# Kernel tuning notes

Measured on AMD Instinct MI355X. Metric: run time of the kernel, lower is better.

Reference implementation:

```python
import jax, jax.numpy as jnp
import numpy as np

B, IN, OUT, K = 16384, 2048, 2048, 8
P, Q = OUT // K, IN // K
W_BIT, IN_BIT = 8, 8
V_MAX = 2.0
ACT_THRES = 6.0


def _ste(base, quantized):
    # straight-through estimator: forward = quantized, backward = d(base)
    return base + jax.lax.stop_gradient(quantized - base)


def quantize_input(x, in_bit):
    # unsigned uniform quantization of activations into [0, 1]
    levels = float(2 ** in_bit - 1)
    xc = jnp.clip(x, 0.0, 1.0)
    xq = jnp.round(xc * levels) / levels
    return _ste(xc, xq)


def quantize_weight(w, w_bit, v_max):
    # symmetric uniform quantization into [-v_max, v_max]
    s = float(2 ** (w_bit - 1) - 1)
    wc = jnp.clip(w, -v_max, v_max)
    wq = jnp.round(wc / v_max * s) / s * v_max
    return _ste(wc, wq)


def setup_inputs() -> dict:
    key = jax.random.key(0)
    k1, k2 = jax.random.split(key)
    x = jax.random.uniform(k1, (B, IN), dtype=jnp.float32)
    weight = jax.random.normal(k2, (P, Q, K, K), dtype=jnp.float32) * 0.1
    return {"x": x, "weight": weight}


def reference(x, weight):
    xq = quantize_input(x, IN_BIT)                    # [B, IN]
    wq = quantize_weight(weight, W_BIT, V_MAX)        # [P, Q, K, K]
    xb = xq.reshape(x.shape[0], Q, K)                 # [B, Q, K]
    # blocked matmul: out[b,p,o] = sum_q sum_i W[p,q,o,i] * x[b,q,i]
    out = jnp.einsum("bqi,pqoi->bpo", xb, wq).reshape(x.shape[0], OUT)
    out = out * out                                   # photodetect: intensity |.|^2
    out = jnp.clip(out, 0.0, ACT_THRES)               # ReLUN(6)
    return out
```

## Files before the change

### kernel.cpp

```cpp
#include <hip/hip_runtime.h>
#include <stdint.h>


typedef int i32x4 __attribute__((ext_vector_type(4)));

#define B_DIM   16384
#define IN_DIM  2048
#define OUT_DIM 2048

#define BM 256
#define BN 256
#define BK 64
#define KTILES (IN_DIM / BK)
#define BUFB   (2 * BM * BK)

__device__ __forceinline__ void async16(const void* g, void* l) {
    __builtin_amdgcn_global_load_lds(
        (const __attribute__((address_space(1))) void*)g,
        (__attribute__((address_space(3))) void*)l, 16, 0, 0);
}

__global__ __launch_bounds__(256) void quant_x_kernel(const float* __restrict__ x,
                                                      int8_t* __restrict__ xq) {
    int i = blockIdx.x * 256 + threadIdx.x;
    const float4* xv = (const float4*)x + (size_t)i * 4;
    union { int8_t c[16]; i32x4 v; } u;
#pragma unroll
    for (int j = 0; j < 4; ++j) {
        float4 v = xv[j];
        float f[4] = {v.x, v.y, v.z, v.w};
#pragma unroll
        for (int e = 0; e < 4; ++e) {
            float c = fminf(fmaxf(f[e], 0.0f), 1.0f);
            int q = (int)rintf(c * 255.0f) - 128;
            u.c[j * 4 + e] = (int8_t)q;
        }
    }
    *((i32x4*)xq + i) = u.v;
}

__global__ __launch_bounds__(256) void quant_w_kernel(const float* __restrict__ w,
                                                      int8_t* __restrict__ wq,
                                                      int* __restrict__ rowsum) {
    int p = blockIdx.x;
    int t = threadIdx.x;
    const float* wp = w + (size_t)p * 16384;
    int n = p * 8 + (t & 7);
    int lsum = 0;
#pragma unroll
    for (int s = 0; s < 8; ++s) {
        int g = t + s * 256;
        float4 v0 = *(const float4*)(wp + g * 8);
        float4 v1 = *(const float4*)(wp + g * 8 + 4);
        float f[8] = {v0.x, v0.y, v0.z, v0.w, v1.x, v1.y, v1.z, v1.w};
        union { int8_t c[8]; long long ll; } u;
#pragma unroll
        for (int e = 0; e < 8; ++e) {
            float c = fminf(fmaxf(f[e], -2.0f), 2.0f);
            int q = (int)rintf(c * 63.5f);
            u.c[e] = (int8_t)q;
            lsum += q;
        }
        int kg = g >> 3;
        *(long long*)(wq + (size_t)n * 2048 + kg * 8) = u.ll;
    }
    atomicAdd(&rowsum[n], lsum);
}

__global__ __launch_bounds__(512, 2) void gemm_i8_kernel(const int8_t* __restrict__ A,
                                                         const int8_t* __restrict__ W,
                                                         const int* __restrict__ rowsum,
                                                         float* __restrict__ out) {
    extern __shared__ int8_t lds[];

    int bid = blockIdx.x;
    int wg = (bid & 7) * 64 + (bid >> 3);
    int tm = wg >> 3;
    int tn = wg & 7;
    int brow = tm * BM;
    int bcol = tn * BN;

    int tid  = threadIdx.x;
    int lane = tid & 63;
    int wv   = tid >> 6;
    int wr = wv >> 2, wc = wv & 3;
    int l15 = lane & 15;
    int kg  = lane >> 4;

    int r0 = tid >> 2;
    int c0 = tid & 3;
    int sw = ((c0 ^ ((r0 >> 1) & 3)) << 4);
    const int8_t* gA0 = A + (size_t)(brow + r0) * IN_DIM + sw;
    const int8_t* gA1 = A + (size_t)(brow + r0 + 128) * IN_DIM + sw;
    const int8_t* gB0 = W + (size_t)(bcol + r0) * IN_DIM + sw;
    const int8_t* gB1 = W + (size_t)(bcol + r0 + 128) * IN_DIM + sw;
    const int ldsOff = tid * 16;

    const int koff = ((kg ^ ((l15 >> 1) & 3)) << 4);
    const int aoff = (wr * 128 + l15) * BK + koff;
    const int boff = (wc * 64 + l15) * BK + koff;

    i32x4 acc[8][4];
#pragma unroll
    for (int m = 0; m < 8; ++m)
#pragma unroll
        for (int n = 0; n < 4; ++n)
            acc[m][n] = (i32x4){0, 0, 0, 0};

    auto stage = [&](int bi, int kt) {
        int8_t* la = lds + bi * BUFB;
        int8_t* lb = la + BM * BK;
        const int kb = kt * BK;
        async16(gA0 + kb, la + ldsOff);
        async16(gA1 + kb, la + ldsOff + 8192);
        async16(gB0 + kb, lb + ldsOff);
        async16(gB1 + kb, lb + ldsOff + 8192);
    };

    auto compute = [&](int bi) {
        const int8_t* la = lds + bi * BUFB;
        const int8_t* lb = la + BM * BK;
        i32x4 af[8], bf[4];
#pragma unroll
        for (int m = 0; m < 8; ++m)
            af[m] = *(const i32x4*)(la + aoff + m * (16 * BK));
#pragma unroll
        for (int n = 0; n < 4; ++n)
            bf[n] = *(const i32x4*)(lb + boff + n * (16 * BK));
#pragma unroll
        for (int m = 0; m < 8; ++m)
#pragma unroll
            for (int n = 0; n < 4; ++n)
                acc[m][n] = __builtin_amdgcn_mfma_i32_16x16x64_i8(af[m], bf[n],
                                                                  acc[m][n], 0, 0, 0);
    };

    stage(0, 0);
    stage(1, 1);

    for (int kt = 0; kt < KTILES - 2; ++kt) {
        asm volatile("s_waitcnt vmcnt(4)" ::: "memory");
        __builtin_amdgcn_s_barrier();
        __builtin_amdgcn_sched_barrier(0);
        stage((kt + 2) % 3, kt + 2);
        compute(kt % 3);
    }
    asm volatile("s_waitcnt vmcnt(4)" ::: "memory");
    __builtin_amdgcn_s_barrier();
    __builtin_amdgcn_sched_barrier(0);
    compute((KTILES - 2) % 3);
    asm volatile("s_waitcnt vmcnt(0)" ::: "memory");
    __builtin_amdgcn_s_barrier();
    __builtin_amdgcn_sched_barrier(0);
    compute((KTILES - 1) % 3);

    const float scale = (float)(2.0 / 32385.0);
#pragma unroll
    for (int n = 0; n < 4; ++n) {
        int col = bcol + wc * 64 + n * 16 + l15;
        int rs128 = rowsum[col] << 7;
#pragma unroll
        for (int m = 0; m < 8; ++m) {
            int row0 = brow + wr * 128 + m * 16 + kg * 4;
#pragma unroll
            for (int r = 0; r < 4; ++r) {
                float f = (float)(acc[m][n][r] + rs128) * scale;
                f = f * f;
                f = fminf(f, 6.0f);
                out[(size_t)(row0 + r) * OUT_DIM + col] = f;
            }
        }
    }
}

extern "C" void kernel_launch(void* const* d_in, const int* in_sizes, int n_in,
                              void* d_out, int out_size, void* d_ws, size_t ws_size,
                              hipStream_t stream) {
    const float* x  = (const float*)d_in[0];
    const float* wt = (const float*)d_in[1];
    float* out = (float*)d_out;

    char* ws = (char*)d_ws;
    int8_t* xq = (int8_t*)ws;
    int8_t* wq = (int8_t*)(ws + (size_t)B_DIM * IN_DIM);
    int*    rowsum = (int*)(ws + (size_t)B_DIM * IN_DIM
                               + (size_t)OUT_DIM * IN_DIM);

    hipMemsetAsync(rowsum, 0, OUT_DIM * sizeof(int), stream);
    quant_x_kernel<<<(B_DIM * IN_DIM / 16) / 256, 256, 0, stream>>>(x, xq);
    quant_w_kernel<<<256, 256, 0, stream>>>(wt, wq, rowsum);
    gemm_i8_kernel<<<(B_DIM / BM) * (OUT_DIM / BN), 512, 3 * BUFB, stream>>>(xq, wq, rowsum, out);
}
```

Before: 125.2 us.

## Split each K-tile into two phases, interleaving LDS reads, async loads and MFMAs

Restructures the int8 GEMM main loop into a ping-pong style schedule. Each K-tile is computed in two halves: A/B fragments for the first half are read, the A prefetch is issued, then MFMAs run at raised priority, followed by the second half with the B prefetch. The loop is unrolled by three to make buffer indices compile-time constants. This is meant to overlap LDS reads and global loads with matrix math and to cut fragment register pressure, at the cost of extra barriers per tile.

```diff
diff --git a/kernel.cpp b/kernel.cpp
--- a/kernel.cpp
+++ b/kernel.cpp
@@ -67,6 +67,59 @@
     atomicAdd(&rowsum[n], lsum);
 }
 
+#define MFMA_I8(a, b, c) __builtin_amdgcn_mfma_i32_16x16x64_i8(a, b, c, 0, 0, 0)
+
+#define DO_TILE(BI, KT2, STG, WAITN) do {                                     \
+    int8_t* la = lds + (BI) * BUFB;                                           \
+    int8_t* lb = la + BM * BK;                                                \
+    int8_t* ldst = lds + (((BI) + 2) % 3) * BUFB;                             \
+            \
+    _Pragma("unroll")                                                         \
+    for (int m = 0; m < 4; ++m)                                               \
+        af[m] = *(const i32x4*)(la + aoff + m * 1024);                        \
+    _Pragma("unroll")                                                         \
+    for (int n = 0; n < 4; ++n)                                               \
+        bf[n] = *(const i32x4*)(lb + boff + n * 1024);                        \
+    if (STG) { const int kb = (KT2) * BK;                                     \
+        async16(gA0 + kb, ldst + ldsOff);                                     \
+        async16(gA1 + kb, ldst + ldsOff + 8192); }                            \
+    __builtin_amdgcn_sched_barrier(0);                                        \
+    __builtin_amdgcn_s_barrier();                                             \
+    asm volatile("s_waitcnt lgkmcnt(0)" ::: "memory");                        \
+    __builtin_amdgcn_sched_barrier(0);                                        \
+    __builtin_amdgcn_s_setprio(1);                                            \
+    _Pragma("unroll")                                                         \
+    for (int m = 0; m < 4; ++m)                                               \
+        _Pragma("unroll")                                                     \
+        for (int n = 0; n < 4; ++n)                                           \
+            acc[m][n] = MFMA_I8(af[m], bf[n], acc[m][n]);                     \
+    __builtin_amdgcn_s_setprio(0);                                            \
+    __builtin_amdgcn_sched_barrier(0);                                        \
+    __builtin_amdgcn_s_barrier();                                             \
+                  \
+    _Pragma("unroll")                                                         \
+    for (int m = 4; m < 8; ++m)                                               \
+        af[m] = *(const i32x4*)(la + aoff + m * 1024);                        \
+    if (STG) { const int kb = (KT2) * BK;                                     \
+        async16(gB0 + kb, ldst + BM * BK + ldsOff);                           \
+        async16(gB1 + kb, ldst + BM * BK + ldsOff + 8192); }                  \
+    __builtin_amdgcn_sched_barrier(0);                                        \
+    __builtin_amdgcn_s_barrier();                                             \
+    asm volatile("s_waitcnt lgkmcnt(0)" ::: "memory");                        \
+    __builtin_amdgcn_sched_barrier(0);                                        \
+    __builtin_amdgcn_s_setprio(1);                                            \
+    _Pragma("unroll")                                                         \
+    for (int m = 4; m < 8; ++m)                                               \
+        _Pragma("unroll")                                                     \
+        for (int n = 0; n < 4; ++n)                                           \
+            acc[m][n] = MFMA_I8(af[m], bf[n], acc[m][n]);                     \
+    __builtin_amdgcn_s_setprio(0);                                            \
+    __builtin_amdgcn_sched_barrier(0);                                        \
+    if ((WAITN) == 4)      asm volatile("s_waitcnt vmcnt(4)" ::: "memory");   \
+    else if ((WAITN) == 0) asm volatile("s_waitcnt vmcnt(0)" ::: "memory");   \
+    if ((WAITN) >= 0) __builtin_amdgcn_s_barrier();                           \
+} while (0)
+
 __global__ __launch_bounds__(512, 2) void gemm_i8_kernel(const int8_t* __restrict__ A,
                                                          const int8_t* __restrict__ W,
                                                          const int* __restrict__ rowsum,
@@ -106,53 +159,29 @@
 #pragma unroll
         for (int n = 0; n < 4; ++n)
             acc[m][n] = (i32x4){0, 0, 0, 0};
-
-    auto stage = [&](int bi, int kt) {
-        int8_t* la = lds + bi * BUFB;
-        int8_t* lb = la + BM * BK;
-        const int kb = kt * BK;
-        async16(gA0 + kb, la + ldsOff);
-        async16(gA1 + kb, la + ldsOff + 8192);
-        async16(gB0 + kb, lb + ldsOff);
-        async16(gB1 + kb, lb + ldsOff + 8192);
-    };
-
-    auto compute = [&](int bi) {
-        const int8_t* la = lds + bi * BUFB;
-        const int8_t* lb = la + BM * BK;
-        i32x4 af[8], bf[4];
-#pragma unroll
-        for (int m = 0; m < 8; ++m)
-            af[m] = *(const i32x4*)(la + aoff + m * (16 * BK));
-#pragma unroll
-        for (int n = 0; n < 4; ++n)
-            bf[n] = *(const i32x4*)(lb + boff + n * (16 * BK));
-#pragma unroll
-        for (int m = 0; m < 8; ++m)
-#pragma unroll
-            for (int n = 0; n < 4; ++n)
-                acc[m][n] = __builtin_amdgcn_mfma_i32_16x16x64_i8(af[m], bf[n],
-                                                                  acc[m][n], 0, 0, 0);
-    };
-
-    stage(0, 0);
-    stage(1, 1);
-
-    for (int kt = 0; kt < KTILES - 2; ++kt) {
-        asm volatile("s_waitcnt vmcnt(4)" ::: "memory");
-        __builtin_amdgcn_s_barrier();
-        __builtin_amdgcn_sched_barrier(0);
-        stage((kt + 2) % 3, kt + 2);
-        compute(kt % 3);
-    }
+    i32x4 af[8], bf[4];
+
+    async16(gA0, lds + ldsOff);
+    async16(gA1, lds + ldsOff + 8192);
+    async16(gB0, lds + BM * BK + ldsOff);
+    async16(gB1, lds + BM * BK + ldsOff + 8192);
+    async16(gA0 + BK, lds + BUFB + ldsOff);
+    async16(gA1 + BK, lds + BUFB + ldsOff + 8192);
+    async16(gB0 + BK, lds + BUFB + BM * BK + ldsOff);
+    async16(gB1 + BK, lds + BUFB + BM * BK + ldsOff + 8192);
     asm volatile("s_waitcnt vmcnt(4)" ::: "memory");
     __builtin_amdgcn_s_barrier();
-    __builtin_amdgcn_sched_barrier(0);
-    compute((KTILES - 2) % 3);
-    asm volatile("s_waitcnt vmcnt(0)" ::: "memory");
-    __builtin_amdgcn_s_barrier();
-    __builtin_amdgcn_sched_barrier(0);
-    compute((KTILES - 1) % 3);
+
+    int kt = 0;
+#pragma unroll 1
+    for (int t = 0; t < 10; ++t) {
+        DO_TILE(0, kt + 2, 1, 4);
+        DO_TILE(1, kt + 3, 1, 4);
+        DO_TILE(2, kt + 4, 1, 4);
+        kt += 3;
+    }
+    DO_TILE(0, 0, 0, 0);
+    DO_TILE(1, 0, 0, -1);
 
     const float scale = (float)(2.0 / 32385.0);
 #pragma unroll
```

After: 123.1 us. About the same (-1.7%).

## Fuse activation quantization into int8 GEMM A-tile loading with interleaved MFMA schedule

Applied to the files above, without the earlier changes.

Removes the separate x-quantization kernel. The GEMM now loads fp32 activations into registers, quantizes them to int8 in-kernel and writes them to LDS. Weight tiles still arrive through async global-to-LDS loads. The main loop is also restructured: LDS fragment reads are interleaved with MFMA groups under explicit waitcnts, the MFMA section runs at raised wave priority, and the loop is unrolled over three buffers. This avoids the extra int8 round trip through memory and one launch, but each column tile now re-reads fp32 activations, which is four times the bytes per tile, and the extra VALU quantization work competes with the MFMAs.

```diff
diff --git a/kernel.cpp b/kernel.cpp
--- a/kernel.cpp
+++ b/kernel.cpp
@@ -12,7 +12,8 @@
 #define BN 256
 #define BK 64
 #define KTILES (IN_DIM / BK)
-#define BUFB   (2 * BM * BK)
+#define ATILE  (BM * BK)
+#define BUFB   (2 * ATILE)
 
 __device__ __forceinline__ void async16(const void* g, void* l) {
     __builtin_amdgcn_global_load_lds(
@@ -20,23 +21,12 @@
         (__attribute__((address_space(3))) void*)l, 16, 0, 0);
 }
 
-__global__ __launch_bounds__(256) void quant_x_kernel(const float* __restrict__ x,
-                                                      int8_t* __restrict__ xq) {
-    int i = blockIdx.x * 256 + threadIdx.x;
-    const float4* xv = (const float4*)x + (size_t)i * 4;
-    union { int8_t c[16]; i32x4 v; } u;
-#pragma unroll
-    for (int j = 0; j < 4; ++j) {
-        float4 v = xv[j];
-        float f[4] = {v.x, v.y, v.z, v.w};
-#pragma unroll
-        for (int e = 0; e < 4; ++e) {
-            float c = fminf(fmaxf(f[e], 0.0f), 1.0f);
-            int q = (int)rintf(c * 255.0f) - 128;
-            u.c[j * 4 + e] = (int8_t)q;
-        }
-    }
-    *((i32x4*)xq + i) = u.v;
+__device__ __forceinline__ int q4(float4 v) {
+    int a = (int)rintf(fminf(fmaxf(v.x, 0.f), 1.f) * 255.f) - 128;
+    int b = (int)rintf(fminf(fmaxf(v.y, 0.f), 1.f) * 255.f) - 128;
+    int c = (int)rintf(fminf(fmaxf(v.z, 0.f), 1.f) * 255.f) - 128;
+    int d = (int)rintf(fminf(fmaxf(v.w, 0.f), 1.f) * 255.f) - 128;
+    return (a & 255) | ((b & 255) << 8) | ((c & 255) << 16) | ((d & 255) << 24);
 }
 
 __global__ __launch_bounds__(256) void quant_w_kernel(const float* __restrict__ w,
@@ -67,7 +57,73 @@
     atomicAdd(&rowsum[n], lsum);
 }
 
-__global__ __launch_bounds__(512, 2) void gemm_i8_kernel(const int8_t* __restrict__ A,
+#define SB0 __builtin_amdgcn_sched_barrier(0)
+#define WLG(n) asm volatile("s_waitcnt lgkmcnt(" #n ")" ::: "memory")
+#define WVM(n) asm volatile("s_waitcnt vmcnt(" #n ")" ::: "memory")
+
+#define CL(mm)                                                                \
+    _Pragma("unroll")                                                         \
+    for (int n = 0; n < 4; ++n)                                               \
+        acc[mm][n] = __builtin_amdgcn_mfma_i32_16x16x64_i8(af[mm], bf[n],     \
+                                                           acc[mm][n], 0, 0, 0);
+
+#define DO_TILE(BI, KT2, STG, TAILW) do {                                     \
+    const int8_t* la = lds + (BI) * BUFB;                                     \
+    const int8_t* lb = la + ATILE;                                            \
+    int8_t* dst = lds + (((BI) + 2) % 3) * BUFB;                              \
+    if (STG) {            \
+        const float* g0 = gx0 + (size_t)(KT2) * BK;                           \
+        const float* g1 = gx1 + (size_t)(KT2) * BK;                           \
+        fa0 = *(const float4*)(g0);       fa1 = *(const float4*)(g0 + 4);     \
+        fa2 = *(const float4*)(g0 + 8);   fa3 = *(const float4*)(g0 + 12);    \
+        fa4 = *(const float4*)(g1);       fa5 = *(const float4*)(g1 + 4);     \
+        fa6 = *(const float4*)(g1 + 8);   fa7 = *(const float4*)(g1 + 12);    \
+    }                                                                         \
+    SB0;                                                                      \
+    if (STG) {            \
+        async16(gB0 + (KT2) * BK, dst + ATILE + ldsOff);                      \
+        async16(gB1 + (KT2) * BK, dst + ATILE + ldsOff + 8192);               \
+    }                                                                         \
+    SB0;                                                                      \
+    bf[0] = *(const i32x4*)(lb + boff);                                       \
+    bf[1] = *(const i32x4*)(lb + boff + 1024);                                \
+    bf[2] = *(const i32x4*)(lb + boff + 2048);                                \
+    bf[3] = *(const i32x4*)(lb + boff + 3072);                                \
+    af[0] = *(const i32x4*)(la + aoff);                                       \
+    SB0;                                                                      \
+    af[1] = *(const i32x4*)(la + aoff + 1024);                                \
+    af[2] = *(const i32x4*)(la + aoff + 2048);                                \
+    SB0;                                                                      \
+    __builtin_amdgcn_s_setprio(1);                                            \
+    WLG(2); SB0; CL(0);                                                       \
+    af[3] = *(const i32x4*)(la + aoff + 3072); SB0;                           \
+    WLG(2); SB0; CL(1);                                                       \
+    af[4] = *(const i32x4*)(la + aoff + 4096); SB0;                           \
+    WLG(2); SB0; CL(2);                                                       \
+    af[5] = *(const i32x4*)(la + aoff + 5120); SB0;                           \
+    WLG(2); SB0; CL(3);                                                       \
+    af[6] = *(const i32x4*)(la + aoff + 6144); SB0;                           \
+    WLG(2); SB0; CL(4);                                                       \
+    af[7] = *(const i32x4*)(la + aoff + 7168); SB0;                           \
+    WLG(2); SB0; CL(5);                                                       \
+    WLG(1); SB0; CL(6);                                                       \
+    WLG(0); SB0; CL(7);                                                       \
+    __builtin_amdgcn_s_setprio(0);                                            \
+    SB0;                                                                      \
+    if (STG) {            \
+        WVM(2); SB0;                                                          \
+        i32x4 pk0, pk1;                                                       \
+        pk0[0] = q4(fa0); pk0[1] = q4(fa1); pk0[2] = q4(fa2); pk0[3] = q4(fa3);\
+        pk1[0] = q4(fa4); pk1[1] = q4(fa5); pk1[2] = q4(fa6); pk1[3] = q4(fa7);\
+        *(i32x4*)(dst + ldsOff) = pk0;                                        \
+        *(i32x4*)(dst + ldsOff + 8192) = pk1;                                 \
+    }                                                                         \
+    if ((TAILW) == 0) { WVM(0); }                                             \
+    WLG(0);                                                                   \
+    __builtin_amdgcn_s_barrier();                                             \
+} while (0)
+
+__global__ __launch_bounds__(512, 2) void gemm_i8_kernel(const float* __restrict__ X,
                                                          const int8_t* __restrict__ W,
                                                          const int* __restrict__ rowsum,
                                                          float* __restrict__ out) {
@@ -90,8 +146,8 @@
     int r0 = tid >> 2;
     int c0 = tid & 3;
     int sw = ((c0 ^ ((r0 >> 1) & 3)) << 4);
-    const int8_t* gA0 = A + (size_t)(brow + r0) * IN_DIM + sw;
-    const int8_t* gA1 = A + (size_t)(brow + r0 + 128) * IN_DIM + sw;
+    const float*  gx0 = X + (size_t)(brow + r0) * IN_DIM + sw;
+    const float*  gx1 = X + (size_t)(brow + r0 + 128) * IN_DIM + sw;
     const int8_t* gB0 = W + (size_t)(bcol + r0) * IN_DIM + sw;
     const int8_t* gB1 = W + (size_t)(bcol + r0 + 128) * IN_DIM + sw;
     const int ldsOff = tid * 16;
@@ -106,53 +162,53 @@
 #pragma unroll
         for (int n = 0; n < 4; ++n)
             acc[m][n] = (i32x4){0, 0, 0, 0};
-
-    auto stage = [&](int bi, int kt) {
-        int8_t* la = lds + bi * BUFB;
-        int8_t* lb = la + BM * BK;
-        const int kb = kt * BK;
-        async16(gA0 + kb, la + ldsOff);
-        async16(gA1 + kb, la + ldsOff + 8192);
-        async16(gB0 + kb, lb + ldsOff);
-        async16(gB1 + kb, lb + ldsOff + 8192);
-    };
-
-    auto compute = [&](int bi) {
-        const int8_t* la = lds + bi * BUFB;
-        const int8_t* lb = la + BM * BK;
-        i32x4 af[8], bf[4];
-#pragma unroll
-        for (int m = 0; m < 8; ++m)
-            af[m] = *(const i32x4*)(la + aoff + m * (16 * BK));
-#pragma unroll
-        for (int n = 0; n < 4; ++n)
-            bf[n] = *(const i32x4*)(lb + boff + n * (16 * BK));
-#pragma unroll
-        for (int m = 0; m < 8; ++m)
-#pragma unroll
-            for (int n = 0; n < 4; ++n)
-                acc[m][n] = __builtin_amdgcn_mfma_i32_16x16x64_i8(af[m], bf[n],
-                                                                  acc[m][n], 0, 0, 0);
-    };
-
-    stage(0, 0);
-    stage(1, 1);
-
-    for (int kt = 0; kt < KTILES - 2; ++kt) {
-        asm volatile("s_waitcnt vmcnt(4)" ::: "memory");
-        __builtin_amdgcn_s_barrier();
-        __builtin_amdgcn_sched_barrier(0);
-        stage((kt + 2) % 3, kt + 2);
-        compute(kt % 3);
-    }
-    asm volatile("s_waitcnt vmcnt(4)" ::: "memory");
+    i32x4 af[8], bf[4];
+    float4 fa0, fa1, fa2, fa3, fa4, fa5, fa6, fa7;
+
+    fa0 = *(const float4*)(gx0);      fa1 = *(const float4*)(gx0 + 4);
+    fa2 = *(const float4*)(gx0 + 8);  fa3 = *(const float4*)(gx0 + 12);
+    fa4 = *(const float4*)(gx1);      fa5 = *(const float4*)(gx1 + 4);
+    fa6 = *(const float4*)(gx1 + 8);  fa7 = *(const float4*)(gx1 + 12);
+    SB0;
+    async16(gB0, lds + ATILE + ldsOff);
+    async16(gB1, lds + ATILE + ldsOff + 8192);
+    async16(gB0 + BK, lds + BUFB + ATILE + ldsOff);
+    async16(gB1 + BK, lds + BUFB + ATILE + ldsOff + 8192);
+    SB0;
+    WVM(4); SB0;
+    {
+        i32x4 pk0, pk1;
+        pk0[0] = q4(fa0); pk0[1] = q4(fa1); pk0[2] = q4(fa2); pk0[3] = q4(fa3);
+        pk1[0] = q4(fa4); pk1[1] = q4(fa5); pk1[2] = q4(fa6); pk1[3] = q4(fa7);
+        *(i32x4*)(lds + ldsOff) = pk0;
+        *(i32x4*)(lds + ldsOff + 8192) = pk1;
+    }
+    fa0 = *(const float4*)(gx0 + BK);      fa1 = *(const float4*)(gx0 + BK + 4);
+    fa2 = *(const float4*)(gx0 + BK + 8);  fa3 = *(const float4*)(gx0 + BK + 12);
+    fa4 = *(const float4*)(gx1 + BK);      fa5 = *(const float4*)(gx1 + BK + 4);
+    fa6 = *(const float4*)(gx1 + BK + 8);  fa7 = *(const float4*)(gx1 + BK + 12);
+    SB0;
+    WVM(0); SB0;
+    {
+        i32x4 pk0, pk1;
+        pk0[0] = q4(fa0); pk0[1] = q4(fa1); pk0[2] = q4(fa2); pk0[3] = q4(fa3);
+        pk1[0] = q4(fa4); pk1[1] = q4(fa5); pk1[2] = q4(fa6); pk1[3] = q4(fa7);
+        *(i32x4*)(lds + BUFB + ldsOff) = pk0;
+        *(i32x4*)(lds + BUFB + ldsOff + 8192) = pk1;
+    }
+    WLG(0);
     __builtin_amdgcn_s_barrier();
-    __builtin_amdgcn_sched_barrier(0);
-    compute((KTILES - 2) % 3);
-    asm volatile("s_waitcnt vmcnt(0)" ::: "memory");
-    __builtin_amdgcn_s_barrier();
-    __builtin_amdgcn_sched_barrier(0);
-    compute((KTILES - 1) % 3);
+
+    int kt = 0;
+#pragma unroll 1
+    for (int t = 0; t < 10; ++t) {
+        DO_TILE(0, kt + 2, 1, 2);
+        DO_TILE(1, kt + 3, 1, 2);
+        DO_TILE(2, kt + 4, 1, 2);
+        kt += 3;
+    }
+    DO_TILE(0, 0, 0, 0);
+    DO_TILE(1, 0, 0, -1);
 
     const float scale = (float)(2.0 / 32385.0);
 #pragma unroll
@@ -181,13 +237,10 @@
     float* out = (float*)d_out;
 
     char* ws = (char*)d_ws;
-    int8_t* xq = (int8_t*)ws;
-    int8_t* wq = (int8_t*)(ws + (size_t)B_DIM * IN_DIM);
-    int*    rowsum = (int*)(ws + (size_t)B_DIM * IN_DIM
-                               + (size_t)OUT_DIM * IN_DIM);
+    int8_t* wq = (int8_t*)ws;
+    int*    rowsum = (int*)(ws + (size_t)OUT_DIM * IN_DIM);
 
     hipMemsetAsync(rowsum, 0, OUT_DIM * sizeof(int), stream);
-    quant_x_kernel<<<(B_DIM * IN_DIM / 16) / 256, 256, 0, stream>>>(x, xq);
     quant_w_kernel<<<256, 256, 0, stream>>>(wt, wq, rowsum);
-    gemm_i8_kernel<<<(B_DIM / BM) * (OUT_DIM / BN), 512, 3 * BUFB, stream>>>(xq, wq, rowsum, out);
-}
+    gemm_i8_kernel<<<(B_DIM / BM) * (OUT_DIM / BN), 512, 3 * BUFB, stream>>>(x, wq, rowsum, out);
+}
```

After: 187.4 us. 1.5x slower.

## Restructure int8 GEMM main loop into double-buffered BK=128 phased schedule

Applied to the files above, without the earlier changes.

Doubles the K tile to 128 and replaces the triple-buffered stage/compute loop with a double-buffered scheme. Each tile is split into four phases that interleave LDS fragment reads, async global-to-LDS loads of the next tile, barriers and MFMA bursts raised with s_setprio. The LDS swizzle is widened to eight 16-byte chunks to match the new row width. The aim is to hide load latency behind MFMA work and cut per-iteration barrier overhead. In exchange it adds many more barriers and lgkm waits per tile and a full vmcnt(0) drain at the end of each tile, which could stall the pipeline.

```diff
diff --git a/kernel.cpp b/kernel.cpp
--- a/kernel.cpp
+++ b/kernel.cpp
@@ -10,9 +10,10 @@
 
 #define BM 256
 #define BN 256
-#define BK 64
+#define BK 128
 #define KTILES (IN_DIM / BK)
-#define BUFB   (2 * BM * BK)
+#define ATILE  (BM * BK)
+#define BUFB   (2 * ATILE)
 
 __device__ __forceinline__ void async16(const void* g, void* l) {
     __builtin_amdgcn_global_load_lds(
@@ -67,6 +68,78 @@
     atomicAdd(&rowsum[n], lsum);
 }
 
+#define SB0 __builtin_amdgcn_sched_barrier(0)
+#define BAR __builtin_amdgcn_s_barrier()
+#define WLG0 asm volatile("s_waitcnt lgkmcnt(0)" ::: "memory")
+#define WVM0 asm volatile("s_waitcnt vmcnt(0)" ::: "memory")
+
+#define CL(mm)                                                                \
+    _Pragma("unroll")                                                         \
+    for (int n = 0; n < 4; ++n)                                               \
+        acc[mm][n] = __builtin_amdgcn_mfma_i32_16x16x64_i8(af[mm], bf[n],     \
+                                                           acc[mm][n], 0, 0, 0);
+
+#define DO_TILE(BI, KT2, STG) do {                                            \
+    const int8_t* la = lds + (BI) * BUFB;                                     \
+    const int8_t* lb = la + ATILE;                                            \
+    int8_t* dst = lds + ((BI) ^ 1) * BUFB;                                    \
+    const int kb = (KT2) * BK;                                                \
+                                             \
+    af[0] = *(const i32x4*)(la + aoff0);                                      \
+    af[1] = *(const i32x4*)(la + aoff0 + 2048);                               \
+    af[2] = *(const i32x4*)(la + aoff0 + 4096);                               \
+    af[3] = *(const i32x4*)(la + aoff0 + 6144);                               \
+    bf[0] = *(const i32x4*)(lb + boff0);                                      \
+    bf[1] = *(const i32x4*)(lb + boff0 + 2048);                               \
+    bf[2] = *(const i32x4*)(lb + boff0 + 4096);                               \
+    bf[3] = *(const i32x4*)(lb + boff0 + 6144);                               \
+    if (STG) { async16(gA + kb,          dst + ldsOff);                       \
+               async16(gA + 131072 + kb, dst + 8192 + ldsOff); }              \
+    SB0; BAR; WLG0; SB0;                                                      \
+    __builtin_amdgcn_s_setprio(1);                                            \
+    CL(0); CL(1); CL(2); CL(3);                                               \
+    __builtin_amdgcn_s_setprio(0); SB0; BAR;                                  \
+                                             \
+    af[4] = *(const i32x4*)(la + aoff0 + 8192);                               \
+    af[5] = *(const i32x4*)(la + aoff0 + 10240);                              \
+    af[6] = *(const i32x4*)(la + aoff0 + 12288);                              \
+    af[7] = *(const i32x4*)(la + aoff0 + 14336);                              \
+    if (STG) { async16(gA + 262144 + kb, dst + 16384 + ldsOff);               \
+               async16(gA + 393216 + kb, dst + 24576 + ldsOff); }             \
+    SB0; BAR; WLG0; SB0;                                                      \
+    __builtin_amdgcn_s_setprio(1);                                            \
+    CL(4); CL(5); CL(6); CL(7);                                               \
+    __builtin_amdgcn_s_setprio(0); SB0; BAR;                                  \
+                                             \
+    af[0] = *(const i32x4*)(la + aoff1);                                      \
+    af[1] = *(const i32x4*)(la + aoff1 + 2048);                               \
+    af[2] = *(const i32x4*)(la + aoff1 + 4096);                               \
+    af[3] = *(const i32x4*)(la + aoff1 + 6144);                               \
+    bf[0] = *(const i32x4*)(lb + boff1);                                      \
+    bf[1] = *(const i32x4*)(lb + boff1 + 2048);                               \
+    bf[2] = *(const i32x4*)(lb + boff1 + 4096);                               \
+    bf[3] = *(const i32x4*)(lb + boff1 + 6144);                               \
+    if (STG) { async16(gB + kb,          dst + ATILE + ldsOff);               \
+               async16(gB + 131072 + kb, dst + ATILE + 8192 + ldsOff); }      \
+    SB0; BAR; WLG0; SB0;                                                      \
+    __builtin_amdgcn_s_setprio(1);                                            \
+    CL(0); CL(1); CL(2); CL(3);                                               \
+    __builtin_amdgcn_s_setprio(0); SB0; BAR;                                  \
+                                             \
+    af[4] = *(const i32x4*)(la + aoff1 + 8192);                               \
+    af[5] = *(const i32x4*)(la + aoff1 + 10240);                              \
+    af[6] = *(const i32x4*)(la + aoff1 + 12288);                              \
+    af[7] = *(const i32x4*)(la + aoff1 + 14336);                              \
+    if (STG) { async16(gB + 262144 + kb, dst + ATILE + 16384 + ldsOff);       \
+               async16(gB + 393216 + kb, dst + ATILE + 24576 + ldsOff); }     \
+    SB0; BAR; WLG0; SB0;                                                      \
+    __builtin_amdgcn_s_setprio(1);                                            \
+    CL(4); CL(5); CL(6); CL(7);                                               \
+    __builtin_amdgcn_s_setprio(0); SB0;                                       \
+    if (STG) { WVM0; }                                                        \
+    BAR;                                                                      \
+} while (0)
+
 __global__ __launch_bounds__(512, 2) void gemm_i8_kernel(const int8_t* __restrict__ A,
                                                          const int8_t* __restrict__ W,
                                                          const int* __restrict__ rowsum,
@@ -87,18 +160,19 @@
     int l15 = lane & 15;
     int kg  = lane >> 4;
 
-    int r0 = tid >> 2;
-    int c0 = tid & 3;
-    int sw = ((c0 ^ ((r0 >> 1) & 3)) << 4);
-    const int8_t* gA0 = A + (size_t)(brow + r0) * IN_DIM + sw;
-    const int8_t* gA1 = A + (size_t)(brow + r0 + 128) * IN_DIM + sw;
-    const int8_t* gB0 = W + (size_t)(bcol + r0) * IN_DIM + sw;
-    const int8_t* gB1 = W + (size_t)(bcol + r0 + 128) * IN_DIM + sw;
+    int t8  = tid >> 3;
+    int csw = (tid & 7) ^ ((tid >> 4) & 7);
+    const int8_t* gA = A + (size_t)(brow + t8) * IN_DIM + csw * 16;
+    const int8_t* gB = W + (size_t)(bcol + t8) * IN_DIM + csw * 16;
     const int ldsOff = tid * 16;
 
-    const int koff = ((kg ^ ((l15 >> 1) & 3)) << 4);
-    const int aoff = (wr * 128 + l15) * BK + koff;
-    const int boff = (wc * 64 + l15) * BK + koff;
+    const int xsw   = (l15 >> 1) & 7;
+    const int koff0 = ((kg ^ xsw) << 4);
+    const int koff1 = (((4 + kg) ^ xsw) << 4);
+    const int arp = (wr * 128 + l15) * BK;
+    const int brp = (wc * 64 + l15) * BK;
+    const int aoff0 = arp + koff0, aoff1 = arp + koff1;
+    const int boff0 = brp + koff0, boff1 = brp + koff1;
 
     i32x4 acc[8][4];
 #pragma unroll
@@ -106,53 +180,26 @@
 #pragma unroll
         for (int n = 0; n < 4; ++n)
             acc[m][n] = (i32x4){0, 0, 0, 0};
-
-    auto stage = [&](int bi, int kt) {
-        int8_t* la = lds + bi * BUFB;
-        int8_t* lb = la + BM * BK;
-        const int kb = kt * BK;
-        async16(gA0 + kb, la + ldsOff);
-        async16(gA1 + kb, la + ldsOff + 8192);
-        async16(gB0 + kb, lb + ldsOff);
-        async16(gB1 + kb, lb + ldsOff + 8192);
-    };
-
-    auto compute = [&](int bi) {
-        const int8_t* la = lds + bi * BUFB;
-        const int8_t* lb = la + BM * BK;
-        i32x4 af[8], bf[4];
-#pragma unroll
-        for (int m = 0; m < 8; ++m)
-            af[m] = *(const i32x4*)(la + aoff + m * (16 * BK));
-#pragma unroll
-        for (int n = 0; n < 4; ++n)
-            bf[n] = *(const i32x4*)(lb + boff + n * (16 * BK));
-#pragma unroll
-        for (int m = 0; m < 8; ++m)
-#pragma unroll
-            for (int n = 0; n < 4; ++n)
-                acc[m][n] = __builtin_amdgcn_mfma_i32_16x16x64_i8(af[m], bf[n],
-                                                                  acc[m][n], 0, 0, 0);
-    };
-
-    stage(0, 0);
-    stage(1, 1);
-
-    for (int kt = 0; kt < KTILES - 2; ++kt) {
-        asm volatile("s_waitcnt vmcnt(4)" ::: "memory");
-        __builtin_amdgcn_s_barrier();
-        __builtin_amdgcn_sched_barrier(0);
-        stage((kt + 2) % 3, kt + 2);
-        compute(kt % 3);
-    }
-    asm volatile("s_waitcnt vmcnt(4)" ::: "memory");
-    __builtin_amdgcn_s_barrier();
-    __builtin_amdgcn_sched_barrier(0);
-    compute((KTILES - 2) % 3);
-    asm volatile("s_waitcnt vmcnt(0)" ::: "memory");
-    __builtin_amdgcn_s_barrier();
-    __builtin_amdgcn_sched_barrier(0);
-    compute((KTILES - 1) % 3);
+    i32x4 af[8], bf[4];
+
+    async16(gA,          lds + ldsOff);
+    async16(gA + 131072, lds + 8192 + ldsOff);
+    async16(gA + 262144, lds + 16384 + ldsOff);
+    async16(gA + 393216, lds + 24576 + ldsOff);
+    async16(gB,          lds + ATILE + ldsOff);
+    async16(gB + 131072, lds + ATILE + 8192 + ldsOff);
+    async16(gB + 262144, lds + ATILE + 16384 + ldsOff);
+    async16(gB + 393216, lds + ATILE + 24576 + ldsOff);
+    SB0; WVM0; BAR;
+
+#pragma unroll 1
+    for (int t = 0; t < 7; ++t) {
+        int kt = 2 * t;
+        DO_TILE(0, kt + 1, 1);
+        DO_TILE(1, kt + 2, 1);
+    }
+    DO_TILE(0, 15, 1);
+    DO_TILE(1, 0, 0);
 
     const float scale = (float)(2.0 / 32385.0);
 #pragma unroll
@@ -189,5 +236,5 @@
     hipMemsetAsync(rowsum, 0, OUT_DIM * sizeof(int), stream);
     quant_x_kernel<<<(B_DIM * IN_DIM / 16) / 256, 256, 0, stream>>>(x, xq);
     quant_w_kernel<<<256, 256, 0, stream>>>(wt, wq, rowsum);
-    gemm_i8_kernel<<<(B_DIM / BM) * (OUT_DIM / BN), 512, 3 * BUFB, stream>>>(xq, wq, rowsum, out);
-}
+    gemm_i8_kernel<<<(B_DIM / BM) * (OUT_DIM / BN), 512, 2 * BUFB, stream>>>(xq, wq, rowsum, out);
+}
```

After: 121.7 us. 1.03x faster.
